# Kernel optimization log

Measured on AMD Instinct MI355X. Metric: run time of the kernel, lower is better.

The kernel has to match this reference:

```python
import jax, jax.numpy as jnp
import numpy as np

ALPHA = 0.5  # mixing weight between dot-product and wedge-norm terms


def setup_inputs() -> dict:
    key = jax.random.key(0)
    kq, kk, kv = jax.random.split(key, 3)
    B, L, H, E = 2, 2048, 8, 32
    queries = jax.random.normal(kq, (B, L, H, E), dtype=jnp.float32)
    keys = jax.random.normal(kk, (B, L, H, E), dtype=jnp.float32)
    values = jax.random.normal(kv, (B, L, H, E), dtype=jnp.float32)
    return {"queries": queries, "keys": keys, "values": values}


def reference(queries, keys, values):
    # queries: [B,L,H,E], keys: [B,S,H,E], values: [B,S,H,D]
    E = queries.shape[-1]
    scale = 1.0 / jnp.sqrt(jnp.asarray(E, dtype=queries.dtype))
    # dot product scores: [B,H,L,S]
    dot = jnp.einsum('blhe,bshe->bhls', queries, keys)
    # squared norms -> broadcastable [B,H,L,1] and [B,H,1,S]
    qn2 = jnp.sum(queries ** 2, axis=-1).transpose(0, 2, 1)[..., :, None]
    kn2 = jnp.sum(keys ** 2, axis=-1).transpose(0, 2, 1)[..., None, :]
    # wedge (Clifford) squared norm, clamped at 0
    wedge = jax.nn.relu(qn2 * kn2 - dot ** 2)
    scores = (ALPHA * dot - (1.0 - ALPHA) * wedge) * scale
    attn = jax.nn.softmax(scores, axis=-1)  # [B,H,L,S]
    # out: [B,L,H,D]
    out = jnp.einsum('bhls,bshd->blhd', attn, values)
    return out
```

## Files before the change

kernel.cpp:

```cpp
#include <hip/hip_runtime.h>
#include <hip/hip_bf16.h>
#include <math.h>


#define NB 2
#define NL 2048
#define NS 2048
#define NH 8
#define NBH 16
#define CSC 0.12751742f

#define WS_KN2_OFF 0u
#define WS_KHKL_OFF 131072u
#define WS_VT_OFF (131072u + 4194304u)
#define WS_PACC_OFF (131072u + 4194304u + 2097152u)
#define WS_PML_OFF (WS_PACC_OFF + 16777216u)
#define WS_NEED (WS_PML_OFF + 1048576u)

typedef float f32x4 __attribute__((ext_vector_type(4)));
typedef short s16x8 __attribute__((ext_vector_type(8)));
typedef unsigned short u16;

__device__ inline unsigned pk2(float a, float b) {
    __hip_bfloat162 t = __float22bfloat162_rn(make_float2(a, b));
    union { __hip_bfloat162 h; unsigned u; } cv;
    cv.h = t;
    return cv.u;
}
template <int CTRL>
__device__ inline float dpp_add(float x) {
    return x + __int_as_float(__builtin_amdgcn_mov_dpp(__float_as_int(x), CTRL, 0xF, 0xF, false));
}
__device__ inline void dma16(const void* gp, void* lp) {
    __builtin_amdgcn_global_load_lds(
        (__attribute__((address_space(1))) void*)(void*)gp,
        (__attribute__((address_space(3))) void*)lp, 16, 0, 0);
}
__device__ inline int swzK(int row) { return (row ^ (row >> 2)) & 3; }
__device__ inline int swzV(int row) { return (row + (row >> 3)) & 7; }

__global__ __launch_bounds__(256) void ga_pre(const float* __restrict__ K,
                                              const float* __restrict__ V,
                                              float* __restrict__ kn2w,
                                              u16* __restrict__ khkl,
                                              u16* __restrict__ vtw) {
    __shared__ float Vf[64][36];
    const int T = threadIdx.x;
    const int bh = blockIdx.x >> 5, stile = blockIdx.x & 31;
    const int b = bh >> 3, h = bh & 7;
    const int s0 = stile * 64;
    const int sk = T >> 2, kc = T & 3;

    const float* kp = K + ((size_t)((b * NS + s0 + sk) * NH + h)) * 32 + kc * 8;
    float4 f0 = *(const float4*)kp, f1 = *(const float4*)(kp + 4);
    float kx[8] = {f0.x, f0.y, f0.z, f0.w, f1.x, f1.y, f1.z, f1.w};
    unsigned hh[4], ll[4];
    float kn2p = 0.f;
#pragma unroll
    for (int i = 0; i < 4; i++) {
        float x0 = kx[2 * i], x1 = kx[2 * i + 1];
        kn2p = fmaf(x0, x0, kn2p);
        kn2p = fmaf(x1, x1, kn2p);
        unsigned h01 = pk2(x0, x1);
        hh[i] = h01;
        float h0 = __uint_as_float(h01 << 16);
        float h1 = __uint_as_float(h01 & 0xffff0000u);
        ll[i] = pk2(x0 - h0, x1 - h1);
    }
    u16* kd = khkl + ((size_t)(bh * NS + s0 + sk)) * 64;
    const int swk = sk & 7;
    *(uint4*)(kd + ((kc ^ swk) * 8)) = make_uint4(hh[0], hh[1], hh[2], hh[3]);
    *(uint4*)(kd + (((4 + kc) ^ swk) * 8)) = make_uint4(ll[0], ll[1], ll[2], ll[3]);
    kn2p = dpp_add<0xB1>(kn2p);
    kn2p = dpp_add<0x4E>(kn2p);
    if (kc == 0) kn2w[bh * NS + s0 + sk] = kn2p;

    const float* vp = V + ((size_t)((b * NS + s0 + sk) * NH + h)) * 32 + kc * 8;
    float4 g0 = *(const float4*)vp, g1 = *(const float4*)(vp + 4);
    *(float4*)&Vf[sk][kc * 8] = g0;
    *(float4*)&Vf[sk][kc * 8 + 4] = g1;
    __syncthreads();
    const int dr = T >> 3, c = T & 7;
    float vv[8];
#pragma unroll
    for (int i = 0; i < 8; i++) vv[i] = Vf[c * 8 + i][dr];
    const int phys = c ^ (dr & 7);
    *(uint4*)(vtw + ((size_t)(bh * 32 + dr)) * NS + s0 + phys * 8) =
        make_uint4(pk2(vv[0], vv[1]), pk2(vv[2], vv[3]), pk2(vv[4], vv[5]), pk2(vv[6], vv[7]));
}

__global__ __launch_bounds__(256, 4) void ga_dma(
    const float* __restrict__ Q, const float* __restrict__ kn2w,
    const u16* __restrict__ khkl, const u16* __restrict__ vtw,
    float* __restrict__ pacc, float* __restrict__ pml) {
    __shared__ u16 sK[2][64][64];
    __shared__ u16 sV[2][32][64];
    __shared__ u16 sP[4][16][64];

    const int T = threadIdx.x;
    const int lane = T & 63, wave = T >> 6;
    const int g = lane >> 4, lc = lane & 15, g8 = g * 8;
    const int blk = blockIdx.x;
    const int qt = blk & 31, strip = (blk >> 5) & 3, bh = blk >> 7;
    const int b = bh >> 3, h = bh & 7;
    const int qw = qt * 64 + wave * 16;
    const int kb0 = strip * 512;

    const float* qrow = Q + ((size_t)((b * NL + qw + lc) * NH + h)) * 32 + g8;
    float4 qa = *(const float4*)qrow, qb = *(const float4*)(qrow + 4);
    float q8[8] = {qa.x, qa.y, qa.z, qa.w, qb.x, qb.y, qb.z, qb.w};
    union { unsigned u4[4]; s16x8 v; } qh_, ql_;
    float qn2 = 0.f;
#pragma unroll
    for (int i = 0; i < 4; i++) {
        float x0 = q8[2 * i], x1 = q8[2 * i + 1];
        qn2 = fmaf(x0, x0, qn2);
        qn2 = fmaf(x1, x1, qn2);
        unsigned h01 = pk2(x0, x1);
        qh_.u4[i] = h01;
        float h0 = __uint_as_float(h01 << 16);
        float h1 = __uint_as_float(h01 & 0xffff0000u);
        ql_.u4[i] = pk2(x0 - h0, x1 - h1);
    }
    const s16x8 qh = qh_.v, ql = ql_.v;
    qn2 += __shfl_xor(qn2, 16);
    qn2 += __shfl_xor(qn2, 32);

    const char* ksrc = (const char*)khkl +
        ((size_t)(bh * NS + kb0 + 16 * wave)) * 128 + lane * 16;
    const char* vsrc = (const char*)vtw +
        ((size_t)(bh * 32 + 8 * wave + (lane >> 3))) * (NS * 2) +
        (size_t)(kb0 + (lane & 7) * 8) * 2;
    const float* kn2b = kn2w + (size_t)bh * NS + kb0;

    dma16(ksrc, &sK[0][16 * wave][0]);
    dma16(ksrc + 1024, &sK[0][16 * wave + 8][0]);
    dma16(vsrc, &sV[0][8 * wave][0]);
    __syncthreads();

    s16x8 ones;
#pragma unroll
    for (int i = 0; i < 8; i++) ones[i] = (short)0x3F80;

    f32x4 acc0 = {0.f, 0.f, 0.f, 0.f}, acc1 = {0.f, 0.f, 0.f, 0.f};
    float m = -1e30f, l = 0.f;
    const f32x4 z = {0.f, 0.f, 0.f, 0.f};
    const int sw = lc & 7;

    for (int t = 0; t < 8; ++t) {
        const int cur = t & 1;
        if (t + 1 < 8) {
            const char* k2 = ksrc + (size_t)(t + 1) * 8192;
            const char* v2 = vsrc + (size_t)(t + 1) * 128;
            dma16(k2, &sK[cur ^ 1][16 * wave][0]);
            dma16(k2 + 1024, &sK[cur ^ 1][16 * wave + 8][0]);
            dma16(v2, &sV[cur ^ 1][8 * wave][0]);
        }
        const int kl64 = t * 64;

        f32x4 d[4], kn2v[4];
#pragma unroll
        for (int st = 0; st < 4; st++) {
            kn2v[st] = *(const f32x4*)(kn2b + kl64 + 16 * st + 4 * g);
            s16x8 kh = *(s16x8*)&sK[cur][16 * st + lc][(g ^ sw) * 8];
            s16x8 klo = *(s16x8*)&sK[cur][16 * st + lc][((4 + g) ^ sw) * 8];
            f32x4 dd = __builtin_amdgcn_mfma_f32_16x16x32_bf16(klo, qh, z, 0, 0, 0);
            dd = __builtin_amdgcn_mfma_f32_16x16x32_bf16(kh, ql, dd, 0, 0, 0);
            dd = __builtin_amdgcn_mfma_f32_16x16x32_bf16(kh, qh, dd, 0, 0, 0);
            d[st] = dd;
        }
        s16x8 va0 = *(s16x8*)&sV[cur][lc][(g ^ sw) * 8];
        s16x8 va1 = *(s16x8*)&sV[cur][lc][((4 + g) ^ sw) * 8];
        s16x8 va2 = *(s16x8*)&sV[cur][lc + 16][(g ^ sw) * 8];
        s16x8 va3 = *(s16x8*)&sV[cur][lc + 16][((4 + g) ^ sw) * 8];

        float sc[4][4];
#pragma unroll
        for (int st = 0; st < 4; st++)
#pragma unroll
            for (int r = 0; r < 4; r++) {
                float dd = d[st][r];
                float c = qn2 * kn2v[st][r];
                sc[st][r] = fminf(dd, fmaf(dd, dd, -c) + dd);
            }

        float x0 = fmaxf(fmaxf(sc[0][0], sc[0][1]), fmaxf(sc[0][2], sc[0][3]));
        float x1 = fmaxf(fmaxf(sc[1][0], sc[1][1]), fmaxf(sc[1][2], sc[1][3]));
        float x2 = fmaxf(fmaxf(sc[2][0], sc[2][1]), fmaxf(sc[2][2], sc[2][3]));
        float x3 = fmaxf(fmaxf(sc[3][0], sc[3][1]), fmaxf(sc[3][2], sc[3][3]));
        float tm = fmaxf(fmaxf(x0, x1), fmaxf(x2, x3));
        tm = fmaxf(tm, __shfl_xor(tm, 16));
        tm = fmaxf(tm, __shfl_xor(tm, 32));
        const float nm = fmaxf(m, tm);
        const float negmC = -nm * CSC;
        const float al = __builtin_amdgcn_exp2f(fmaf(m, CSC, negmC));
        m = nm;
        float p[4][4];
#pragma unroll
        for (int st = 0; st < 4; st++)
#pragma unroll
            for (int r = 0; r < 4; r++)
                p[st][r] = __builtin_amdgcn_exp2f(fmaf(sc[st][r], CSC, negmC));

#pragma unroll
        for (int st = 0; st < 4; st++) {
            const int off = (((2 * st + (g >> 1)) ^ sw) << 3) + ((g & 1) << 2);
            *(uint2*)&sP[wave][lc][off] =
                make_uint2(pk2(p[st][0], p[st][1]), pk2(p[st][2], p[st][3]));
        }
        __builtin_amdgcn_s_waitcnt(0xC07F);
        s16x8 pb0 = *(s16x8*)&sP[wave][lc][(g ^ sw) * 8];
        s16x8 pb1 = *(s16x8*)&sP[wave][lc][((4 + g) ^ sw) * 8];

        acc0 *= al;
        acc1 *= al;
        acc0 = __builtin_amdgcn_mfma_f32_16x16x32_bf16(va0, pb0, acc0, 0, 0, 0);
        acc0 = __builtin_amdgcn_mfma_f32_16x16x32_bf16(va1, pb1, acc0, 0, 0, 0);
        acc1 = __builtin_amdgcn_mfma_f32_16x16x32_bf16(va2, pb0, acc1, 0, 0, 0);
        acc1 = __builtin_amdgcn_mfma_f32_16x16x32_bf16(va3, pb1, acc1, 0, 0, 0);
        f32x4 lt = __builtin_amdgcn_mfma_f32_16x16x32_bf16(ones, pb0, z, 0, 0, 0);
        lt = __builtin_amdgcn_mfma_f32_16x16x32_bf16(ones, pb1, lt, 0, 0, 0);
        l = fmaf(l, al, lt[0]);

        __syncthreads();
    }

    float* pa = pacc + (((size_t)bh * 4 + strip) * NL + (qw + lc)) * 32;
    *(f32x4*)(pa + 4 * g) = acc0;
    *(f32x4*)(pa + 16 + 4 * g) = acc1;
    if (g == 0) {
        *(float2*)(pml + (((size_t)bh * 4 + strip) * NL + (qw + lc)) * 2) =
            make_float2(m, l);
    }
}

__global__ __launch_bounds__(256) void ga_combine(const float* __restrict__ pacc,
                                                  const float* __restrict__ pml,
                                                  float* __restrict__ O) {
    const int tid = blockIdx.x * 256 + threadIdx.x;
    const int dq = tid & 7, q = (tid >> 3) & 2047, bh = tid >> 14;
    const int b = bh >> 3, h = bh & 7;
    float m[4], l[4];
#pragma unroll
    for (int s = 0; s < 4; s++) {
        float2 t = *(const float2*)(pml + (((size_t)bh * 4 + s) * NL + q) * 2);
        m[s] = t.x;
        l[s] = t.y;
    }
    float mf = fmaxf(fmaxf(m[0], m[1]), fmaxf(m[2], m[3]));
    float w[4], L = 0.f;
#pragma unroll
    for (int s = 0; s < 4; s++) {
        w[s] = __builtin_amdgcn_exp2f((m[s] - mf) * CSC);
        L = fmaf(l[s], w[s], L);
    }
    const float inv = 1.f / L;
    float4 o = make_float4(0.f, 0.f, 0.f, 0.f);
#pragma unroll
    for (int s = 0; s < 4; s++) {
        const float* pa = pacc + (((size_t)bh * 4 + s) * NL + q) * 32 + dq * 4;
        float4 a = *(const float4*)pa;
        o.x = fmaf(a.x, w[s], o.x);
        o.y = fmaf(a.y, w[s], o.y);
        o.z = fmaf(a.z, w[s], o.z);
        o.w = fmaf(a.w, w[s], o.w);
    }
    o.x *= inv; o.y *= inv; o.z *= inv; o.w *= inv;
    *(float4*)(O + (((size_t)(b * NL + q)) * NH + h) * 32 + dq * 4) = o;
}

__global__ __launch_bounds__(512, 4) void ga_fallback(
    const float* __restrict__ Q, const float* __restrict__ K,
    const float* __restrict__ V, float* __restrict__ O) {
    __shared__ union {
        struct {
            u16 Kh[2][64][32];
            u16 Kl[2][64][32];
            u16 Vt[2][32][64];
            float kn2[2][64];
        } s;
        struct { float acc[8][32][17]; float m[8][16]; float l[8][16]; } c;
    } u;
    __shared__ u16 sP[8][16][64];

    const int T = threadIdx.x;
    const int lane = T & 63, wave = T >> 6;
    const int g = lane >> 4, lc = lane & 15, g8 = g * 8;
    const int half = wave >> 2;
    const int qt = blockIdx.x & 31;
    const int bh = blockIdx.x >> 5;
    const int b = bh >> 3, h = bh & 7;
    const int qw = qt * 64 + (wave & 3) * 16;

    const float* qrow = Q + ((size_t)((b * NL + qw + lc) * NH + h)) * 32 + g8;
    float4 qa = *(const float4*)qrow, qb = *(const float4*)(qrow + 4);
    float q8[8] = {qa.x, qa.y, qa.z, qa.w, qb.x, qb.y, qb.z, qb.w};
    union { unsigned u4[4]; s16x8 v; } qh_, ql_;
    float qn2 = 0.f;
#pragma unroll
    for (int i = 0; i < 4; i++) {
        float x0 = q8[2 * i], x1 = q8[2 * i + 1];
        qn2 = fmaf(x0, x0, qn2);
        qn2 = fmaf(x1, x1, qn2);
        unsigned h01 = pk2(x0, x1);
        qh_.u4[i] = h01;
        float h0 = __uint_as_float(h01 << 16);
        float h1 = __uint_as_float(h01 & 0xffff0000u);
        ql_.u4[i] = pk2(x0 - h0, x1 - h1);
    }
    const s16x8 qh = qh_.v, ql = ql_.v;
    qn2 += __shfl_xor(qn2, 16);
    qn2 += __shfl_xor(qn2, 32);

    const int Tl = T & 255;
    const int sk = Tl >> 2, kc = Tl & 3;
    const int dv = Tl & 31, vc = Tl >> 5;
    const float* kbase = K + ((size_t)(b * NS * NH) + h) * 32;
    const float* vbase = V + ((size_t)(b * NS * NH) + h) * 32;
    const int kphys = (kc ^ swzK(sk)) * 8;
    const int vphys = (vc ^ swzV(dv)) * 8;

    int s0 = half * 1024;
    float4 ka = *(const float4*)(kbase + (size_t)(s0 + sk) * 256 + kc * 8);
    float4 kb = *(const float4*)(kbase + (size_t)(s0 + sk) * 256 + kc * 8 + 4);
    float vr[8];
#pragma unroll
    for (int i = 0; i < 8; i++) vr[i] = vbase[(size_t)(s0 + 8 * vc + i) * 256 + dv];

    f32x4 acc0 = {0.f, 0.f, 0.f, 0.f}, acc1 = {0.f, 0.f, 0.f, 0.f};
    float m = -INFINITY, l = 0.f;

    for (int t = 0; t < 16; ++t) {
        {
            float kx[8] = {ka.x, ka.y, ka.z, ka.w, kb.x, kb.y, kb.z, kb.w};
            unsigned hh[4], ll[4];
            float kn2p = 0.f;
#pragma unroll
            for (int i = 0; i < 4; i++) {
                float x0 = kx[2 * i], x1 = kx[2 * i + 1];
                kn2p = fmaf(x0, x0, kn2p);
                kn2p = fmaf(x1, x1, kn2p);
                unsigned h01 = pk2(x0, x1);
                hh[i] = h01;
                float h0 = __uint_as_float(h01 << 16);
                float h1 = __uint_as_float(h01 & 0xffff0000u);
                ll[i] = pk2(x0 - h0, x1 - h1);
            }
            *(uint4*)&u.s.Kh[half][sk][kphys] = make_uint4(hh[0], hh[1], hh[2], hh[3]);
            *(uint4*)&u.s.Kl[half][sk][kphys] = make_uint4(ll[0], ll[1], ll[2], ll[3]);
            kn2p = dpp_add<0xB1>(kn2p);
            kn2p = dpp_add<0x4E>(kn2p);
            if (kc == 0) u.s.kn2[half][sk] = kn2p;
            *(uint4*)&u.s.Vt[half][dv][vphys] =
                make_uint4(pk2(vr[0], vr[1]), pk2(vr[2], vr[3]),
                           pk2(vr[4], vr[5]), pk2(vr[6], vr[7]));
        }
        const int tn = (t + 1 < 16) ? t + 1 : t;
        const int sn = half * 1024 + tn * 64;
        ka = *(const float4*)(kbase + (size_t)(sn + sk) * 256 + kc * 8);
        kb = *(const float4*)(kbase + (size_t)(sn + sk) * 256 + kc * 8 + 4);
#pragma unroll
        for (int i = 0; i < 8; i++) vr[i] = vbase[(size_t)(sn + 8 * vc + i) * 256 + dv];

        __syncthreads();

        f32x4 d[4], kn2v[4];
        const f32x4 z = {0.f, 0.f, 0.f, 0.f};
        const int skr = swzK(lc);
#pragma unroll
        for (int st = 0; st < 4; st++) {
            kn2v[st] = *(f32x4*)&u.s.kn2[half][16 * st + 4 * g];
            s16x8 kh = *(s16x8*)&u.s.Kh[half][16 * st + lc][(g ^ skr) * 8];
            s16x8 kl = *(s16x8*)&u.s.Kl[half][16 * st + lc][(g ^ skr) * 8];
            f32x4 dd = __builtin_amdgcn_mfma_f32_16x16x32_bf16(kl, qh, z, 0, 0, 0);
            dd = __builtin_amdgcn_mfma_f32_16x16x32_bf16(kh, ql, dd, 0, 0, 0);
            dd = __builtin_amdgcn_mfma_f32_16x16x32_bf16(kh, qh, dd, 0, 0, 0);
            d[st] = dd;
        }

        float sc[4][4];
#pragma unroll
        for (int st = 0; st < 4; st++)
#pragma unroll
            for (int r = 0; r < 4; r++) {
                float dd = d[st][r];
                float w = fmaxf(fmaf(-dd, dd, qn2 * kn2v[st][r]), 0.f);
                sc[st][r] = (dd - w) * CSC;
            }

        float x0 = fmaxf(fmaxf(sc[0][0], sc[0][1]), fmaxf(sc[0][2], sc[0][3]));
        float x1 = fmaxf(fmaxf(sc[1][0], sc[1][1]), fmaxf(sc[1][2], sc[1][3]));
        float x2 = fmaxf(fmaxf(sc[2][0], sc[2][1]), fmaxf(sc[2][2], sc[2][3]));
        float x3 = fmaxf(fmaxf(sc[3][0], sc[3][1]), fmaxf(sc[3][2], sc[3][3]));
        float tm = fmaxf(fmaxf(x0, x1), fmaxf(x2, x3));
        tm = fmaxf(tm, __shfl_xor(tm, 16));
        tm = fmaxf(tm, __shfl_xor(tm, 32));
        const float nm = fmaxf(m, tm);
        const float al = __builtin_amdgcn_exp2f(m - nm);
        m = nm;
        float p[4][4], ls = 0.f;
#pragma unroll
        for (int st = 0; st < 4; st++)
#pragma unroll
            for (int r = 0; r < 4; r++) {
                p[st][r] = __builtin_amdgcn_exp2f(sc[st][r] - nm);
                ls += p[st][r];
            }
        l = fmaf(l, al, ls);
        acc0 *= al;
        acc1 *= al;

#pragma unroll
        for (int st = 0; st < 4; st++) {
            const int off = ((2 * st + (g >> 1)) ^ (lc & 7)) * 8 + (g & 1) * 4;
            *(uint2*)&sP[wave][lc][off] =
                make_uint2(pk2(p[st][0], p[st][1]), pk2(p[st][2], p[st][3]));
        }
        __builtin_amdgcn_s_waitcnt(0xC07F);

        const int svl = swzV(lc), svh = swzV(lc + 16), spl = lc & 7;
        s16x8 va00 = *(s16x8*)&u.s.Vt[half][lc][(g ^ svl) * 8];
        s16x8 va01 = *(s16x8*)&u.s.Vt[half][lc][((4 + g) ^ svl) * 8];
        s16x8 va10 = *(s16x8*)&u.s.Vt[half][lc + 16][(g ^ svh) * 8];
        s16x8 va11 = *(s16x8*)&u.s.Vt[half][lc + 16][((4 + g) ^ svh) * 8];
        s16x8 pb0 = *(s16x8*)&sP[wave][lc][(g ^ spl) * 8];
        s16x8 pb1 = *(s16x8*)&sP[wave][lc][((4 + g) ^ spl) * 8];
        acc0 = __builtin_amdgcn_mfma_f32_16x16x32_bf16(va00, pb0, acc0, 0, 0, 0);
        acc0 = __builtin_amdgcn_mfma_f32_16x16x32_bf16(va01, pb1, acc0, 0, 0, 0);
        acc1 = __builtin_amdgcn_mfma_f32_16x16x32_bf16(va10, pb0, acc1, 0, 0, 0);
        acc1 = __builtin_amdgcn_mfma_f32_16x16x32_bf16(va11, pb1, acc1, 0, 0, 0);

        __syncthreads();
    }

    l += __shfl_xor(l, 16);
    l += __shfl_xor(l, 32);
#pragma unroll
    for (int r = 0; r < 4; r++) {
        u.c.acc[wave][4 * g + r][lc] = acc0[r];
        u.c.acc[wave][16 + 4 * g + r][lc] = acc1[r];
    }
    if (lane < 16) {
        u.c.m[wave][lc] = m;
        u.c.l[wave][lc] = l;
    }
    __syncthreads();

    const int q = T >> 3, dq = (T & 7) * 4, qr = q & 15;
    const int w0 = q >> 4, w1 = w0 + 4;
    float m0 = u.c.m[w0][qr], m1 = u.c.m[w1][qr];
    float l0 = u.c.l[w0][qr], l1 = u.c.l[w1][qr];
    float mf = fmaxf(m0, m1);
    float e0 = __builtin_amdgcn_exp2f(m0 - mf);
    float e1 = __builtin_amdgcn_exp2f(m1 - mf);
    float inv = 1.f / fmaf(l1, e1, l0 * e0);
    e0 *= inv;
    e1 *= inv;
    float4 o;
    o.x = u.c.acc[w0][dq + 0][qr] * e0 + u.c.acc[w1][dq + 0][qr] * e1;
    o.y = u.c.acc[w0][dq + 1][qr] * e0 + u.c.acc[w1][dq + 1][qr] * e1;
    o.z = u.c.acc[w0][dq + 2][qr] * e0 + u.c.acc[w1][dq + 2][qr] * e1;
    o.w = u.c.acc[w0][dq + 3][qr] * e0 + u.c.acc[w1][dq + 3][qr] * e1;
    *(float4*)(O + ((size_t)((b * NL + qt * 64 + q) * NH + h)) * 32 + dq) = o;
}

extern "C" void kernel_launch(void* const* d_in, const int* in_sizes, int n_in,
                              void* d_out, int out_size, void* d_ws, size_t ws_size,
                              hipStream_t stream) {
    const float* Q = (const float*)d_in[0];
    const float* K = (const float*)d_in[1];
    const float* V = (const float*)d_in[2];
    float* O = (float*)d_out;

    if (ws_size >= (size_t)WS_NEED) {
        float* kn2w = (float*)((char*)d_ws + WS_KN2_OFF);
        u16* khkl = (u16*)((char*)d_ws + WS_KHKL_OFF);
        u16* vtw = (u16*)((char*)d_ws + WS_VT_OFF);
        float* pacc = (float*)((char*)d_ws + WS_PACC_OFF);
        float* pml = (float*)((char*)d_ws + WS_PML_OFF);
        ga_pre<<<NBH * 32, 256, 0, stream>>>(K, V, kn2w, khkl, vtw);
        ga_dma<<<NBH * 32 * 4, 256, 0, stream>>>(Q, kn2w, khkl, vtw, pacc, pml);
        ga_combine<<<(NBH * NL * 8) / 256, 256, 0, stream>>>(pacc, pml, O);
    } else {
        ga_fallback<<<NBH * 32, 512, 0, stream>>>(Q, K, V, O);
    }
}
```

Measured before the change: 105.7 us.

## Prefetch kn2 one tile ahead and defer softmax max rescale off critical path

Loads the per-key norm vector for the next tile during the current iteration, so global-load latency is hidden behind compute. Reorders online softmax so exponentials use the previous running max (the first tile's max is computed up front), and the max reduction and rescale of acc and l happen after the PV MFMAs instead of before them. Also writes the score math as two-wide float vectors to encourage packed FP32 instructions. This lifts the cross-lane shuffles and rescale off the dependency chain before the exponentials, at the risk of exp overflow if a later tile's scores far exceed the running max.

```diff
diff --git a/kernel.cpp b/kernel.cpp
--- a/kernel.cpp
+++ b/kernel.cpp
@@ -18,6 +18,7 @@
 #define WS_NEED (WS_PML_OFF + 1048576u)
 
 typedef float f32x4 __attribute__((ext_vector_type(4)));
+typedef float f32x2 __attribute__((ext_vector_type(2)));
 typedef short s16x8 __attribute__((ext_vector_type(8)));
 typedef unsigned short u16;
 
@@ -136,6 +137,9 @@
     dma16(ksrc, &sK[0][16 * wave][0]);
     dma16(ksrc + 1024, &sK[0][16 * wave + 8][0]);
     dma16(vsrc, &sV[0][8 * wave][0]);
+    f32x4 kn2c[4];
+#pragma unroll
+    for (int st = 0; st < 4; st++) kn2c[st] = *(const f32x4*)(kn2b + 16 * st + 4 * g);
     __syncthreads();
 
     s16x8 ones;
@@ -143,25 +147,30 @@
     for (int i = 0; i < 8; i++) ones[i] = (short)0x3F80;
 
     f32x4 acc0 = {0.f, 0.f, 0.f, 0.f}, acc1 = {0.f, 0.f, 0.f, 0.f};
-    float m = -1e30f, l = 0.f;
+    float m_use = 0.f, l = 0.f;
     const f32x4 z = {0.f, 0.f, 0.f, 0.f};
     const int sw = lc & 7;
 
     for (int t = 0; t < 8; ++t) {
         const int cur = t & 1;
-        if (t + 1 < 8) {
-            const char* k2 = ksrc + (size_t)(t + 1) * 8192;
-            const char* v2 = vsrc + (size_t)(t + 1) * 128;
-            dma16(k2, &sK[cur ^ 1][16 * wave][0]);
-            dma16(k2 + 1024, &sK[cur ^ 1][16 * wave + 8][0]);
-            dma16(v2, &sV[cur ^ 1][8 * wave][0]);
-        }
-        const int kl64 = t * 64;
-
-        f32x4 d[4], kn2v[4];
+        f32x4 kn2n[4];
+        {
+            const int tn = (t + 1 < 8) ? t + 1 : t;
+            const char* k2 = ksrc + (size_t)tn * 8192;
+            const char* v2 = vsrc + (size_t)tn * 128;
+            if (t + 1 < 8) {
+                dma16(k2, &sK[cur ^ 1][16 * wave][0]);
+                dma16(k2 + 1024, &sK[cur ^ 1][16 * wave + 8][0]);
+                dma16(v2, &sV[cur ^ 1][8 * wave][0]);
+            }
+#pragma unroll
+            for (int st = 0; st < 4; st++)
+                kn2n[st] = *(const f32x4*)(kn2b + tn * 64 + 16 * st + 4 * g);
+        }
+
+        f32x4 d[4];
 #pragma unroll
         for (int st = 0; st < 4; st++) {
-            kn2v[st] = *(const f32x4*)(kn2b + kl64 + 16 * st + 4 * g);
             s16x8 kh = *(s16x8*)&sK[cur][16 * st + lc][(g ^ sw) * 8];
             s16x8 klo = *(s16x8*)&sK[cur][16 * st + lc][((4 + g) ^ sw) * 8];
             f32x4 dd = __builtin_amdgcn_mfma_f32_16x16x32_bf16(klo, qh, z, 0, 0, 0);
@@ -174,53 +183,63 @@
         s16x8 va2 = *(s16x8*)&sV[cur][lc + 16][(g ^ sw) * 8];
         s16x8 va3 = *(s16x8*)&sV[cur][lc + 16][((4 + g) ^ sw) * 8];
 
-        float sc[4][4];
-#pragma unroll
-        for (int st = 0; st < 4; st++)
-#pragma unroll
-            for (int r = 0; r < 4; r++) {
-                float dd = d[st][r];
-                float c = qn2 * kn2v[st][r];
-                sc[st][r] = fminf(dd, fmaf(dd, dd, -c) + dd);
-            }
-
-        float x0 = fmaxf(fmaxf(sc[0][0], sc[0][1]), fmaxf(sc[0][2], sc[0][3]));
-        float x1 = fmaxf(fmaxf(sc[1][0], sc[1][1]), fmaxf(sc[1][2], sc[1][3]));
-        float x2 = fmaxf(fmaxf(sc[2][0], sc[2][1]), fmaxf(sc[2][2], sc[2][3]));
-        float x3 = fmaxf(fmaxf(sc[3][0], sc[3][1]), fmaxf(sc[3][2], sc[3][3]));
-        float tm = fmaxf(fmaxf(x0, x1), fmaxf(x2, x3));
-        tm = fmaxf(tm, __shfl_xor(tm, 16));
-        tm = fmaxf(tm, __shfl_xor(tm, 32));
-        const float nm = fmaxf(m, tm);
-        const float negmC = -nm * CSC;
-        const float al = __builtin_amdgcn_exp2f(fmaf(m, CSC, negmC));
-        m = nm;
-        float p[4][4];
-#pragma unroll
-        for (int st = 0; st < 4; st++)
-#pragma unroll
-            for (int r = 0; r < 4; r++)
-                p[st][r] = __builtin_amdgcn_exp2f(fmaf(sc[st][r], CSC, negmC));
-
+        f32x2 sc2[4][2];
 #pragma unroll
         for (int st = 0; st < 4; st++) {
+            f32x2 dA = {d[st][0], d[st][1]}, dB = {d[st][2], d[st][3]};
+            f32x2 kA = {kn2c[st][0], kn2c[st][1]}, kB = {kn2c[st][2], kn2c[st][3]};
+            f32x2 tA = dA * dA - qn2 * kA;
+            f32x2 tB = dB * dB - qn2 * kB;
+            f32x2 uA = dA + tA, uB = dB + tB;
+            sc2[st][0] = (f32x2){fminf(dA.x, uA.x), fminf(dA.y, uA.y)};
+            sc2[st][1] = (f32x2){fminf(dB.x, uB.x), fminf(dB.y, uB.y)};
+        }
+
+        f32x2 mx01 = sc2[0][0], mx23 = sc2[0][1];
+#pragma unroll
+        for (int st = 1; st < 4; st++) {
+            mx01 = (f32x2){fmaxf(mx01.x, sc2[st][0].x), fmaxf(mx01.y, sc2[st][0].y)};
+            mx23 = (f32x2){fmaxf(mx23.x, sc2[st][1].x), fmaxf(mx23.y, sc2[st][1].y)};
+        }
+        const float tm = fmaxf(fmaxf(mx01.x, mx01.y), fmaxf(mx23.x, mx23.y));
+        if (t == 0) {
+            float a = fmaxf(tm, __shfl_xor(tm, 16));
+            m_use = fmaxf(a, __shfl_xor(a, 32));
+        }
+        const float negmC = -m_use * CSC;
+
+#pragma unroll
+        for (int st = 0; st < 4; st++) {
+            f32x2 aA = sc2[st][0] * CSC + negmC;
+            f32x2 aB = sc2[st][1] * CSC + negmC;
+            float p0 = __builtin_amdgcn_exp2f(aA.x);
+            float p1 = __builtin_amdgcn_exp2f(aA.y);
+            float p2 = __builtin_amdgcn_exp2f(aB.x);
+            float p3 = __builtin_amdgcn_exp2f(aB.y);
             const int off = (((2 * st + (g >> 1)) ^ sw) << 3) + ((g & 1) << 2);
-            *(uint2*)&sP[wave][lc][off] =
-                make_uint2(pk2(p[st][0], p[st][1]), pk2(p[st][2], p[st][3]));
+            *(uint2*)&sP[wave][lc][off] = make_uint2(pk2(p0, p1), pk2(p2, p3));
         }
         __builtin_amdgcn_s_waitcnt(0xC07F);
         s16x8 pb0 = *(s16x8*)&sP[wave][lc][(g ^ sw) * 8];
         s16x8 pb1 = *(s16x8*)&sP[wave][lc][((4 + g) ^ sw) * 8];
 
-        acc0 *= al;
-        acc1 *= al;
         acc0 = __builtin_amdgcn_mfma_f32_16x16x32_bf16(va0, pb0, acc0, 0, 0, 0);
         acc0 = __builtin_amdgcn_mfma_f32_16x16x32_bf16(va1, pb1, acc0, 0, 0, 0);
         acc1 = __builtin_amdgcn_mfma_f32_16x16x32_bf16(va2, pb0, acc1, 0, 0, 0);
         acc1 = __builtin_amdgcn_mfma_f32_16x16x32_bf16(va3, pb1, acc1, 0, 0, 0);
         f32x4 lt = __builtin_amdgcn_mfma_f32_16x16x32_bf16(ones, pb0, z, 0, 0, 0);
         lt = __builtin_amdgcn_mfma_f32_16x16x32_bf16(ones, pb1, lt, 0, 0, 0);
-        l = fmaf(l, al, lt[0]);
+
+        float a2 = fmaxf(tm, __shfl_xor(tm, 16));
+        float tmx = fmaxf(a2, __shfl_xor(a2, 32));
+        const float mn = fmaxf(m_use, tmx);
+        const float beta = __builtin_amdgcn_exp2f((m_use - mn) * CSC);
+        m_use = mn;
+        l = (l + lt[0]) * beta;
+        acc0 *= beta;
+        acc1 *= beta;
+#pragma unroll
+        for (int st = 0; st < 4; st++) kn2c[st] = kn2n[st];
 
         __syncthreads();
     }
@@ -230,7 +249,7 @@
     *(f32x4*)(pa + 16 + 4 * g) = acc1;
     if (g == 0) {
         *(float2*)(pml + (((size_t)bh * 4 + strip) * NL + (qw + lc)) * 2) =
-            make_float2(m, l);
+            make_float2(m_use, l);
     }
 }
 
```

Measured after the change: 108.1 us. +2.3%, slower.

## Halve key tile to 32 per iteration to double occupancy in attention kernel

Applied to the files above, without the earlier changes.

Shrinks the per-iteration key block from 64 to 32 keys, halving shared-memory buffers for K, V and P. The loop now runs 16 iterations, and the V transpose swizzle is changed to a 4-way pattern within 32-element halves to match the narrower V tile. Launch bounds are raised to 8 blocks per SM to exploit the smaller LDS footprint. The trade-off is more barriers and per-iteration softmax rescale overhead, plus fewer MFMAs between synchronizations.

```diff
diff --git a/kernel.cpp b/kernel.cpp
--- a/kernel.cpp
+++ b/kernel.cpp
@@ -84,18 +84,18 @@
     float vv[8];
 #pragma unroll
     for (int i = 0; i < 8; i++) vv[i] = Vf[c * 8 + i][dr];
-    const int phys = c ^ (dr & 7);
+    const int phys = (c & 4) | ((c & 3) ^ (dr & 3));
     *(uint4*)(vtw + ((size_t)(bh * 32 + dr)) * NS + s0 + phys * 8) =
         make_uint4(pk2(vv[0], vv[1]), pk2(vv[2], vv[3]), pk2(vv[4], vv[5]), pk2(vv[6], vv[7]));
 }
 
-__global__ __launch_bounds__(256, 4) void ga_dma(
+__global__ __launch_bounds__(256, 8) void ga_dma(
     const float* __restrict__ Q, const float* __restrict__ kn2w,
     const u16* __restrict__ khkl, const u16* __restrict__ vtw,
     float* __restrict__ pacc, float* __restrict__ pml) {
-    __shared__ u16 sK[2][64][64];
-    __shared__ u16 sV[2][32][64];
-    __shared__ u16 sP[4][16][64];
+    __shared__ u16 sK[2][32][64];
+    __shared__ u16 sV[2][32][32];
+    __shared__ u16 sP[4][16][32];
 
     const int T = threadIdx.x;
     const int lane = T & 63, wave = T >> 6;
@@ -127,15 +127,14 @@
     qn2 += __shfl_xor(qn2, 32);
 
     const char* ksrc = (const char*)khkl +
-        ((size_t)(bh * NS + kb0 + 16 * wave)) * 128 + lane * 16;
+        ((size_t)(bh * NS + kb0 + 8 * wave)) * 128 + lane * 16;
     const char* vsrc = (const char*)vtw +
-        ((size_t)(bh * 32 + 8 * wave + (lane >> 3))) * (NS * 2) +
-        (size_t)(kb0 + (lane & 7) * 8) * 2;
+        ((size_t)(bh * 32 + 16 * wave + (lane >> 2))) * (NS * 2) +
+        (size_t)(kb0 + (lane & 3) * 8) * 2;
     const float* kn2b = kn2w + (size_t)bh * NS + kb0;
 
-    dma16(ksrc, &sK[0][16 * wave][0]);
-    dma16(ksrc + 1024, &sK[0][16 * wave + 8][0]);
-    dma16(vsrc, &sV[0][8 * wave][0]);
+    dma16(ksrc, &sK[0][8 * wave][0]);
+    if (wave < 2) dma16(vsrc, &sV[0][16 * wave][0]);
     __syncthreads();
 
     s16x8 ones;
@@ -145,23 +144,20 @@
     f32x4 acc0 = {0.f, 0.f, 0.f, 0.f}, acc1 = {0.f, 0.f, 0.f, 0.f};
     float m = -1e30f, l = 0.f;
     const f32x4 z = {0.f, 0.f, 0.f, 0.f};
-    const int sw = lc & 7;
-
-    for (int t = 0; t < 8; ++t) {
+    const int sw = lc & 7, sw4 = lc & 3;
+
+    for (int t = 0; t < 16; ++t) {
         const int cur = t & 1;
-        if (t + 1 < 8) {
-            const char* k2 = ksrc + (size_t)(t + 1) * 8192;
-            const char* v2 = vsrc + (size_t)(t + 1) * 128;
-            dma16(k2, &sK[cur ^ 1][16 * wave][0]);
-            dma16(k2 + 1024, &sK[cur ^ 1][16 * wave + 8][0]);
-            dma16(v2, &sV[cur ^ 1][8 * wave][0]);
-        }
-        const int kl64 = t * 64;
-
-        f32x4 d[4], kn2v[4];
-#pragma unroll
-        for (int st = 0; st < 4; st++) {
-            kn2v[st] = *(const f32x4*)(kn2b + kl64 + 16 * st + 4 * g);
+        if (t + 1 < 16) {
+            dma16(ksrc + (size_t)(t + 1) * 4096, &sK[cur ^ 1][8 * wave][0]);
+            if (wave < 2) dma16(vsrc + (size_t)(t + 1) * 64, &sV[cur ^ 1][16 * wave][0]);
+        }
+        const int kl32 = t * 32;
+
+        f32x4 d[2], kn2v[2];
+#pragma unroll
+        for (int st = 0; st < 2; st++) {
+            kn2v[st] = *(const f32x4*)(kn2b + kl32 + 16 * st + 4 * g);
             s16x8 kh = *(s16x8*)&sK[cur][16 * st + lc][(g ^ sw) * 8];
             s16x8 klo = *(s16x8*)&sK[cur][16 * st + lc][((4 + g) ^ sw) * 8];
             f32x4 dd = __builtin_amdgcn_mfma_f32_16x16x32_bf16(klo, qh, z, 0, 0, 0);
@@ -169,14 +165,12 @@
             dd = __builtin_amdgcn_mfma_f32_16x16x32_bf16(kh, qh, dd, 0, 0, 0);
             d[st] = dd;
         }
-        s16x8 va0 = *(s16x8*)&sV[cur][lc][(g ^ sw) * 8];
-        s16x8 va1 = *(s16x8*)&sV[cur][lc][((4 + g) ^ sw) * 8];
-        s16x8 va2 = *(s16x8*)&sV[cur][lc + 16][(g ^ sw) * 8];
-        s16x8 va3 = *(s16x8*)&sV[cur][lc + 16][((4 + g) ^ sw) * 8];
-
-        float sc[4][4];
-#pragma unroll
-        for (int st = 0; st < 4; st++)
+        s16x8 va0 = *(s16x8*)&sV[cur][lc][(g ^ sw4) * 8];
+        s16x8 va1 = *(s16x8*)&sV[cur][lc + 16][(g ^ sw4) * 8];
+
+        float sc[2][4];
+#pragma unroll
+        for (int st = 0; st < 2; st++)
 #pragma unroll
             for (int r = 0; r < 4; r++) {
                 float dd = d[st][r];
@@ -186,40 +180,34 @@
 
         float x0 = fmaxf(fmaxf(sc[0][0], sc[0][1]), fmaxf(sc[0][2], sc[0][3]));
         float x1 = fmaxf(fmaxf(sc[1][0], sc[1][1]), fmaxf(sc[1][2], sc[1][3]));
-        float x2 = fmaxf(fmaxf(sc[2][0], sc[2][1]), fmaxf(sc[2][2], sc[2][3]));
-        float x3 = fmaxf(fmaxf(sc[3][0], sc[3][1]), fmaxf(sc[3][2], sc[3][3]));
-        float tm = fmaxf(fmaxf(x0, x1), fmaxf(x2, x3));
+        float tm = fmaxf(x0, x1);
         tm = fmaxf(tm, __shfl_xor(tm, 16));
         tm = fmaxf(tm, __shfl_xor(tm, 32));
         const float nm = fmaxf(m, tm);
         const float negmC = -nm * CSC;
         const float al = __builtin_amdgcn_exp2f(fmaf(m, CSC, negmC));
         m = nm;
-        float p[4][4];
-#pragma unroll
-        for (int st = 0; st < 4; st++)
+        float p[2][4];
+#pragma unroll
+        for (int st = 0; st < 2; st++)
 #pragma unroll
             for (int r = 0; r < 4; r++)
                 p[st][r] = __builtin_amdgcn_exp2f(fmaf(sc[st][r], CSC, negmC));
 
 #pragma unroll
-        for (int st = 0; st < 4; st++) {
-            const int off = (((2 * st + (g >> 1)) ^ sw) << 3) + ((g & 1) << 2);
+        for (int st = 0; st < 2; st++) {
+            const int off = (((2 * st + (g >> 1)) ^ sw4) << 3) + ((g & 1) << 2);
             *(uint2*)&sP[wave][lc][off] =
                 make_uint2(pk2(p[st][0], p[st][1]), pk2(p[st][2], p[st][3]));
         }
         __builtin_amdgcn_s_waitcnt(0xC07F);
-        s16x8 pb0 = *(s16x8*)&sP[wave][lc][(g ^ sw) * 8];
-        s16x8 pb1 = *(s16x8*)&sP[wave][lc][((4 + g) ^ sw) * 8];
+        s16x8 pb = *(s16x8*)&sP[wave][lc][(g ^ sw4) * 8];
 
         acc0 *= al;
         acc1 *= al;
-        acc0 = __builtin_amdgcn_mfma_f32_16x16x32_bf16(va0, pb0, acc0, 0, 0, 0);
-        acc0 = __builtin_amdgcn_mfma_f32_16x16x32_bf16(va1, pb1, acc0, 0, 0, 0);
-        acc1 = __builtin_amdgcn_mfma_f32_16x16x32_bf16(va2, pb0, acc1, 0, 0, 0);
-        acc1 = __builtin_amdgcn_mfma_f32_16x16x32_bf16(va3, pb1, acc1, 0, 0, 0);
-        f32x4 lt = __builtin_amdgcn_mfma_f32_16x16x32_bf16(ones, pb0, z, 0, 0, 0);
-        lt = __builtin_amdgcn_mfma_f32_16x16x32_bf16(ones, pb1, lt, 0, 0, 0);
+        acc0 = __builtin_amdgcn_mfma_f32_16x16x32_bf16(va0, pb, acc0, 0, 0, 0);
+        acc1 = __builtin_amdgcn_mfma_f32_16x16x32_bf16(va1, pb, acc1, 0, 0, 0);
+        f32x4 lt = __builtin_amdgcn_mfma_f32_16x16x32_bf16(ones, pb, z, 0, 0, 0);
         l = fmaf(l, al, lt[0]);
 
         __syncthreads();
```

New measurement: 107.6 us. Within noise of the previous version (+1.9%).
